# Performance work log

Hardware: AMD Instinct MI355X
Metric: run time of the kernel (lower is better)

The kernel has to match this reference:

```python
import jax, jax.numpy as jnp
import numpy as np

H = 16        # heads
DH = 64       # dim_head
DM = 1024     # query_dim = context_dim
INNER = H * DH


def setup_inputs() -> dict:
    key = jax.random.key(0)
    ks = jax.random.split(key, 5)
    s = 0.02
    queries = jax.random.normal(ks[0], (2, 2048, DM), dtype=jnp.float32)
    Wq = jax.random.normal(ks[1], (DM, INNER), dtype=jnp.float32) * s
    Wkv = jax.random.normal(ks[2], (DM, 2 * INNER), dtype=jnp.float32) * s
    Wo = jax.random.normal(ks[3], (INNER, DM), dtype=jnp.float32) * s
    bo = jax.random.normal(ks[4], (DM,), dtype=jnp.float32) * s
    return {"queries": queries, "Wq": Wq, "Wkv": Wkv, "Wo": Wo, "bo": bo}


def reference(queries, Wq, Wkv, Wo, bo):
    b, n, _ = queries.shape
    scale = DH ** -0.5
    q = queries @ Wq                       # [b, n, inner]
    kv = queries @ Wkv                     # self-attention: context = queries
    k, v = jnp.split(kv, 2, axis=-1)
    # b n (h d) -> b h n d
    split_heads = lambda t: t.reshape(b, n, H, DH).transpose(0, 2, 1, 3)
    q, k, v = map(split_heads, (q, k, v))
    sim = jnp.einsum('bhid,bhjd->bhij', q, k) * scale
    attn = jax.nn.softmax(sim, axis=-1)    # dropout is identity (p=0 / eval)
    out = jnp.einsum('bhij,bhjd->bhid', attn, v)
    out = out.transpose(0, 2, 1, 3).reshape(b, n, INNER)
    return out @ Wo + bo
```

## Files before the change

### kernel.cpp

```cpp
#include <hip/hip_runtime.h>
#include <math.h>
#include <stdint.h>

typedef _Float16 half8v __attribute__((ext_vector_type(8)));
typedef _Float16 half4v __attribute__((ext_vector_type(4)));
typedef _Float16 half2v __attribute__((ext_vector_type(2)));
typedef __fp16 fp16x2 __attribute__((ext_vector_type(2)));
typedef float floatx4 __attribute__((ext_vector_type(4)));

#define MFMA16(a, b, c) __builtin_amdgcn_mfma_f32_16x16x32_f16(a, b, c, 0, 0, 0)

#define QSCALE 0.18033688011112f

__device__ __forceinline__ void gld_lds16(const void* g, void* l) {
  __builtin_amdgcn_global_load_lds(
      (const __attribute__((address_space(1))) uint32_t*)(uintptr_t)g,
      (__attribute__((address_space(3))) uint32_t*)(uintptr_t)l, 16, 0, 0);
}

__device__ __forceinline__ half2v pk16(float a, float b) {
  fp16x2 t = __builtin_amdgcn_cvt_pkrtz(a, b);
  return __builtin_bit_cast(half2v, t);
}

__global__ __launch_bounds__(256) void prep(
    const float* __restrict__ X, const float* __restrict__ Wq,
    const float* __restrict__ Wkv, const float* __restrict__ Wo,
    _Float16* __restrict__ X16, _Float16* __restrict__ WqkvT,
    _Float16* __restrict__ WoT)
{
  __shared__ alignas(16) _Float16 Tt[64 * 68];
  const int bid = blockIdx.x;
  if (bid < 2048) {
    size_t gid = (size_t)bid * 256 + threadIdx.x;
    const float4* src = (const float4*)(X) + gid * 2;
    float4 a = src[0], b = src[1];
    half8v h;
    h[0]=(_Float16)a.x; h[1]=(_Float16)a.y; h[2]=(_Float16)a.z; h[3]=(_Float16)a.w;
    h[4]=(_Float16)b.x; h[5]=(_Float16)b.y; h[6]=(_Float16)b.z; h[7]=(_Float16)b.w;
    *((half8v*)X16 + gid) = h;
    return;
  }
  int b = bid - 2048;
  const float* src; _Float16* dst; int N, tk, tn;
  if (b < 256)      { src = Wq;  dst = WqkvT;                 N = 1024; tk = b & 15;        tn = b >> 4; }
  else if (b < 768) { src = Wkv; dst = WqkvT + (size_t)1024 * 1024; N = 2048; tk = (b - 256) & 15; tn = (b - 256) >> 4; }
  else              { src = Wo;  dst = WoT;                   N = 1024; tk = (b - 768) & 15; tn = (b - 768) >> 4; }

  const int t = threadIdx.x;
  {
    int kg = t >> 4, ng = t & 15;
    const float* sp = src + (size_t)(tk * 64 + kg * 4) * N + tn * 64 + ng * 4;
    float4 r0 = *(const float4*)(sp);
    float4 r1 = *(const float4*)(sp + N);
    float4 r2 = *(const float4*)(sp + 2 * N);
    float4 r3 = *(const float4*)(sp + 3 * N);
    half4v h;
    h[0]=(_Float16)r0.x; h[1]=(_Float16)r1.x; h[2]=(_Float16)r2.x; h[3]=(_Float16)r3.x;
    *(half4v*)&Tt[(ng * 4 + 0) * 68 + kg * 4] = h;
    h[0]=(_Float16)r0.y; h[1]=(_Float16)r1.y; h[2]=(_Float16)r2.y; h[3]=(_Float16)r3.y;
    *(half4v*)&Tt[(ng * 4 + 1) * 68 + kg * 4] = h;
    h[0]=(_Float16)r0.z; h[1]=(_Float16)r1.z; h[2]=(_Float16)r2.z; h[3]=(_Float16)r3.z;
    *(half4v*)&Tt[(ng * 4 + 2) * 68 + kg * 4] = h;
    h[0]=(_Float16)r0.w; h[1]=(_Float16)r1.w; h[2]=(_Float16)r2.w; h[3]=(_Float16)r3.w;
    *(half4v*)&Tt[(ng * 4 + 3) * 68 + kg * 4] = h;
  }
  __syncthreads();
  #pragma unroll
  for (int i = 0; i < 2; i++) {
    int idx = t + i * 256;
    int nl = idx >> 3, k8 = (idx & 7) * 8;
    half8v v = *(half8v*)&Tt[nl * 68 + k8];
    *(half8v*)(dst + (size_t)(tn * 64 + nl) * 1024 + tk * 64 + k8) = v;
  }
}

__global__ __launch_bounds__(256) void qkv_gemm(
    const _Float16* __restrict__ X16, const _Float16* __restrict__ WqkvT,
    _Float16* __restrict__ q_ws, _Float16* __restrict__ k_ws,
    _Float16* __restrict__ vT_ws)
{
  constexpr int K = 1024;
  __shared__ alignas(16) _Float16 Tt[128 * 136];
  _Float16* As = Tt;
  _Float16* Bs = Tt + 4096;

  const int m0 = blockIdx.x * 128;
  const int n0 = blockIdx.y * 128;

  const int tid  = threadIdx.x;
  const int wave = tid >> 6, lane = tid & 63;
  const int qd = lane >> 4, l15 = lane & 15;
  const int wr = (wave >> 1) * 64, wc = (wave & 1) * 64;
  const int r0i = tid >> 2, c0 = (tid & 3) * 8;

  floatx4 acc[4][4] = {};

  for (int k0 = 0; k0 < K; k0 += 32) {
    gld_lds16(X16 + (size_t)(m0 + r0i) * K + k0 + c0, &As[tid * 8]);
    gld_lds16(X16 + (size_t)(m0 + 64 + r0i) * K + k0 + c0, &As[(tid + 256) * 8]);
    gld_lds16(WqkvT + (size_t)(n0 + r0i) * K + k0 + c0, &Bs[tid * 8]);
    gld_lds16(WqkvT + (size_t)(n0 + 64 + r0i) * K + k0 + c0, &Bs[(tid + 256) * 8]);
    __syncthreads();
    half8v a[4], b[4];
    #pragma unroll
    for (int it = 0; it < 4; it++)
      a[it] = *(half8v*)&As[(wr + it * 16 + l15) * 32 + qd * 8];
    #pragma unroll
    for (int jt = 0; jt < 4; jt++)
      b[jt] = *(half8v*)&Bs[(wc + jt * 16 + l15) * 32 + qd * 8];
    #pragma unroll
    for (int it = 0; it < 4; it++)
      #pragma unroll
      for (int jt = 0; jt < 4; jt++)
        acc[it][jt] = MFMA16(a[it], b[jt], acc[it][jt]);
    __syncthreads();
  }

  if (n0 < 2048) {
    #pragma unroll
    for (int it = 0; it < 4; it++) {
      #pragma unroll
      for (int jt = 0; jt < 4; jt++) {
        #pragma unroll
        for (int r = 0; r < 4; r++) {
          int m = m0 + wr + it * 16 + qd * 4 + r;
          int n = n0 + wc + jt * 16 + l15;
          float val = acc[it][jt][r];
          int bb = m >> 11, nn = m & 2047;
          if (n0 < 1024) {
            int h = n >> 6, d = n & 63;
            q_ws[(((size_t)bb * 16 + h) * 2048 + nn) * 64 + d] = (_Float16)(val * QSCALE);
          } else {
            int c = n - 1024, h = c >> 6, d = c & 63;
            k_ws[(((size_t)bb * 16 + h) * 2048 + nn) * 64 + d] = (_Float16)val;
          }
        }
      }
    }
  } else {
    #pragma unroll
    for (int it = 0; it < 4; it++) {
      #pragma unroll
      for (int jt = 0; jt < 4; jt++) {
        #pragma unroll
        for (int r = 0; r < 4; r++) {
          int ml = wr + it * 16 + qd * 4 + r;
          int nl = wc + jt * 16 + l15;
          Tt[nl * 136 + ml] = (_Float16)acc[it][jt][r];
        }
      }
    }
    __syncthreads();
    int row = tid >> 1;
    int mh  = (tid & 1) * 64;
    int c   = (n0 - 2048) + row;
    int bb  = m0 >> 11;
    int nnb = (m0 & 2047) + mh;
    _Float16* dstp =
        vT_ws + (((size_t)bb * 16 + (c >> 6)) * 64 + (c & 63)) * 2048 + nnb;
    #pragma unroll
    for (int i = 0; i < 8; i++)
      *(half8v*)(dstp + i * 8) = *(half8v*)&Tt[row * 136 + mh + i * 8];
  }
}

__device__ __forceinline__ int swz(int row, int blk) {
  return row * 64 + ((blk ^ (row & 7)) << 3);
}

__global__ __launch_bounds__(128, 2) void attn_kernel(
    const _Float16* __restrict__ q_ws, const _Float16* __restrict__ k_ws,
    const _Float16* __restrict__ vT_ws, _Float16* __restrict__ aout)
{
  constexpr int N = 2048;
  __shared__ alignas(16) _Float16 Qs[64 * 64];
  __shared__ alignas(16) _Float16 Ks[2][64 * 64];
  __shared__ alignas(16) _Float16 Vts[2][64 * 64];

  const int id = blockIdx.x;
  const int bh = ((id >> 8) << 3) | (id & 7);
  const int qt = (id >> 3) & 31;

  const _Float16* Qp = q_ws + (size_t)bh * N * 64;
  const _Float16* Kp = k_ws + (size_t)bh * N * 64;
  const _Float16* Vp = vT_ws + (size_t)bh * 64 * N;

  const int tid = threadIdx.x, wave = tid >> 6, lane = tid & 63;
  const int qd = lane >> 4, l15 = lane & 15;
  const int q0 = qt * 64;
  const int wbase = wave * 32;

  #pragma unroll
  for (int i = 0; i < 4; i++) {
    int idx = tid + i * 128;
    int r = idx >> 3, cb = (idx ^ r) & 7;
    gld_lds16(Qp + (size_t)(q0 + r) * 64 + cb * 8, &Qs[idx * 8]);
    gld_lds16(Kp + (size_t)r * 64 + cb * 8, &Ks[0][idx * 8]);
    gld_lds16(Vp + (size_t)r * N + cb * 8, &Vts[0][idx * 8]);
  }
  __syncthreads();

  half8v qf[2][2];
  #pragma unroll
  for (int m = 0; m < 2; m++)
    #pragma unroll
    for (int ks = 0; ks < 2; ks++)
      qf[m][ks] = *(half8v*)&Qs[swz(wbase + m * 16 + l15, ks * 4 + qd)];

  floatx4 o[2][4] = {};
  float lsum[2] = {};

  int p = 0;
  for (int kv0 = 0; kv0 < N; kv0 += 64) {
    const bool more = (kv0 + 64) < N;
    if (more) {
      int kvn = kv0 + 64;
      #pragma unroll
      for (int i = 0; i < 4; i++) {
        int idx = tid + i * 128;
        int r = idx >> 3, cb = (idx ^ r) & 7;
        gld_lds16(Kp + (size_t)(kvn + r) * 64 + cb * 8, &Ks[p ^ 1][idx * 8]);
        gld_lds16(Vp + (size_t)r * N + kvn + cb * 8, &Vts[p ^ 1][idx * 8]);
      }
    }

    floatx4 s[4][2] = {};
    #pragma unroll
    for (int ks = 0; ks < 2; ks++) {
      half8v kf[4];
      #pragma unroll
      for (int nt = 0; nt < 4; nt++)
        kf[nt] = *(half8v*)&Ks[p][swz(nt * 16 + l15, ks * 4 + qd)];
      #pragma unroll
      for (int nt = 0; nt < 4; nt++)
        #pragma unroll
        for (int m = 0; m < 2; m++)
          s[nt][m] = MFMA16(kf[nt], qf[m][ks], s[nt][m]);
    }

    #pragma unroll
    for (int m = 0; m < 2; m++) {
      #pragma unroll
      for (int nt = 0; nt < 4; nt++) {
        float p0 = __builtin_amdgcn_exp2f(s[nt][m][0]);
        float p1 = __builtin_amdgcn_exp2f(s[nt][m][1]);
        float p2 = __builtin_amdgcn_exp2f(s[nt][m][2]);
        float p3 = __builtin_amdgcn_exp2f(s[nt][m][3]);
        lsum[m] += (p0 + p1) + (p2 + p3);
        half2v h01 = pk16(p0, p1);
        half2v h23 = pk16(p2, p3);
        half4v pk;
        pk[0] = h01[0]; pk[1] = h01[1]; pk[2] = h23[0]; pk[3] = h23[1];
        *(half4v*)&Qs[swz(wbase + m * 16 + l15, 2 * nt + (qd >> 1)) +
                      (qd & 1) * 4] = pk;
      }
    }

    #pragma unroll
    for (int ks = 0; ks < 2; ks++) {
      half8v pf[2], vf[4];
      #pragma unroll
      for (int m = 0; m < 2; m++)
        pf[m] = *(half8v*)&Qs[swz(wbase + m * 16 + l15, 4 * ks + qd)];
      #pragma unroll
      for (int nt = 0; nt < 4; nt++)
        vf[nt] = *(half8v*)&Vts[p][swz(nt * 16 + l15, 4 * ks + qd)];
      #pragma unroll
      for (int m = 0; m < 2; m++)
        #pragma unroll
        for (int nt = 0; nt < 4; nt++)
          o[m][nt] = MFMA16(pf[m], vf[nt], o[m][nt]);
    }

    if (more) __syncthreads();
    p ^= 1;
  }

  #pragma unroll
  for (int m = 0; m < 2; m++) {
    lsum[m] += __shfl_xor(lsum[m], 16);
    lsum[m] += __shfl_xor(lsum[m], 32);
  }

  const int bb = bh >> 4, hh = bh & 15;
  #pragma unroll
  for (int m = 0; m < 2; m++) {
    #pragma unroll
    for (int r = 0; r < 4; r++) {
      float inv = 1.0f / __shfl(lsum[m], qd * 4 + r);
      int n = q0 + wbase + m * 16 + qd * 4 + r;
      #pragma unroll
      for (int dt = 0; dt < 4; dt++) {
        int d = dt * 16 + l15;
        aout[((size_t)(bb * 2048 + n)) * 1024 + hh * 64 + d] =
            (_Float16)(o[m][dt][r] * inv);
      }
    }
  }
}

__global__ __launch_bounds__(256) void out_gemm(
    const _Float16* __restrict__ A, const _Float16* __restrict__ WoT,
    const float* __restrict__ bo, float* __restrict__ Out)
{
  constexpr int K = 1024;
  __shared__ alignas(16) _Float16 As[64 * 32];
  __shared__ alignas(16) _Float16 Bs[128 * 32];

  const int m0 = blockIdx.x * 64;
  const int n0 = blockIdx.y * 128;
  const int tid = threadIdx.x;
  const int wave = tid >> 6, lane = tid & 63;
  const int qd = lane >> 4, l15 = lane & 15;
  const int wr = (wave >> 1) * 32, wc = (wave & 1) * 64;
  const int r0i = tid >> 2, c0 = (tid & 3) * 8;

  floatx4 acc[2][4] = {};

  for (int k0 = 0; k0 < K; k0 += 32) {
    gld_lds16(A + (size_t)(m0 + r0i) * K + k0 + c0, &As[tid * 8]);
    gld_lds16(WoT + (size_t)(n0 + r0i) * K + k0 + c0, &Bs[tid * 8]);
    gld_lds16(WoT + (size_t)(n0 + 64 + r0i) * K + k0 + c0, &Bs[(tid + 256) * 8]);
    __syncthreads();
    half8v a[2], b[4];
    #pragma unroll
    for (int it = 0; it < 2; it++)
      a[it] = *(half8v*)&As[(wr + it * 16 + l15) * 32 + qd * 8];
    #pragma unroll
    for (int jt = 0; jt < 4; jt++)
      b[jt] = *(half8v*)&Bs[(wc + jt * 16 + l15) * 32 + qd * 8];
    #pragma unroll
    for (int it = 0; it < 2; it++)
      #pragma unroll
      for (int jt = 0; jt < 4; jt++)
        acc[it][jt] = MFMA16(a[it], b[jt], acc[it][jt]);
    __syncthreads();
  }

  #pragma unroll
  for (int it = 0; it < 2; it++) {
    #pragma unroll
    for (int jt = 0; jt < 4; jt++) {
      int n = n0 + wc + jt * 16 + l15;
      float bias = bo[n];
      #pragma unroll
      for (int r = 0; r < 4; r++) {
        int m = m0 + wr + it * 16 + qd * 4 + r;
        Out[(size_t)m * 1024 + n] = acc[it][jt][r] + bias;
      }
    }
  }
}

extern "C" void kernel_launch(void* const* d_in, const int* in_sizes, int n_in,
                              void* d_out, int out_size, void* d_ws, size_t ws_size,
                              hipStream_t stream) {
  const float* X   = (const float*)d_in[0];
  const float* Wq  = (const float*)d_in[1];
  const float* Wkv = (const float*)d_in[2];
  const float* Wo  = (const float*)d_in[3];
  const float* bo  = (const float*)d_in[4];
  float* out = (float*)d_out;

  const size_t M4 = (size_t)4 * 1024 * 1024;
  _Float16* q_ws   = (_Float16*)d_ws;
  _Float16* k_ws   = q_ws + M4;
  _Float16* vT_ws  = k_ws + M4;
  _Float16* X16    = vT_ws + M4;
  _Float16* WqkvT  = X16 + M4;
  _Float16* WoT    = WqkvT + (size_t)3 * 1024 * 1024;
  _Float16* aout   = X16;

  prep<<<3072, 256, 0, stream>>>(X, Wq, Wkv, Wo, X16, WqkvT, WoT);
  qkv_gemm<<<dim3(32, 24), 256, 0, stream>>>(X16, WqkvT, q_ws, k_ws, vT_ws);
  attn_kernel<<<1024, 128, 0, stream>>>(q_ws, k_ws, vT_ws, aout);
  out_gemm<<<dim3(64, 8), 256, 0, stream>>>(aout, WoT, bo, out);
}
```

Before: 190.3 us.

## Fuse all four stages into one persistent kernel with grid barriers

Replaces the four separate launches (prep, QKV GEMM, attention, output GEMM) with one persistent kernel of 512 blocks. The stages are separated by atomic-counter grid barriers, and each stage's tiles are mapped onto those blocks. The attention stage now uses 256-thread blocks covering 128 queries each, so 512 blocks replace the previous 1024 of 128 threads. This is meant to remove inter-kernel launch gaps and tail effects. In exchange, the QKV GEMM runs 768 tiles over 512 blocks, which gives an uneven second wave, and it relies on all 512 blocks being co-resident for the spin barrier to be safe.

Result: slower. 389.0 us (+104.4%).

```diff
diff --git a/kernel.cpp b/kernel.cpp
--- a/kernel.cpp
+++ b/kernel.cpp
@@ -23,331 +23,339 @@
   return __builtin_bit_cast(half2v, t);
 }
 
-__global__ __launch_bounds__(256) void prep(
+__device__ __forceinline__ int swz(int row, int blk) {
+  return row * 64 + ((blk ^ (row & 7)) << 3);
+}
+
+__device__ int g_bar;
+
+__device__ __forceinline__ void grid_barrier(int target) {
+  __syncthreads();
+  if (threadIdx.x == 0) {
+    __hip_atomic_fetch_add(&g_bar, 1, __ATOMIC_ACQ_REL,
+                           __HIP_MEMORY_SCOPE_AGENT);
+    while (__hip_atomic_load(&g_bar, __ATOMIC_ACQUIRE,
+                             __HIP_MEMORY_SCOPE_AGENT) < target)
+      __builtin_amdgcn_s_sleep(16);
+  }
+  __syncthreads();
+}
+
+__global__ __launch_bounds__(256, 2) void mega(
     const float* __restrict__ X, const float* __restrict__ Wq,
     const float* __restrict__ Wkv, const float* __restrict__ Wo,
+    const float* __restrict__ bo,
     _Float16* __restrict__ X16, _Float16* __restrict__ WqkvT,
-    _Float16* __restrict__ WoT)
+    _Float16* __restrict__ WoT,
+    _Float16* __restrict__ q_ws, _Float16* __restrict__ k_ws,
+    _Float16* __restrict__ vT_ws,
+    _Float16* __restrict__ aout, float* __restrict__ Out)
 {
-  __shared__ alignas(16) _Float16 Tt[64 * 68];
+  __shared__ alignas(16) _Float16 pool[24576];
   const int bid = blockIdx.x;
-  if (bid < 2048) {
-    size_t gid = (size_t)bid * 256 + threadIdx.x;
-    const float4* src = (const float4*)(X) + gid * 2;
-    float4 a = src[0], b = src[1];
-    half8v h;
-    h[0]=(_Float16)a.x; h[1]=(_Float16)a.y; h[2]=(_Float16)a.z; h[3]=(_Float16)a.w;
-    h[4]=(_Float16)b.x; h[5]=(_Float16)b.y; h[6]=(_Float16)b.z; h[7]=(_Float16)b.w;
-    *((half8v*)X16 + gid) = h;
-    return;
-  }
-  int b = bid - 2048;
-  const float* src; _Float16* dst; int N, tk, tn;
-  if (b < 256)      { src = Wq;  dst = WqkvT;                 N = 1024; tk = b & 15;        tn = b >> 4; }
-  else if (b < 768) { src = Wkv; dst = WqkvT + (size_t)1024 * 1024; N = 2048; tk = (b - 256) & 15; tn = (b - 256) >> 4; }
-  else              { src = Wo;  dst = WoT;                   N = 1024; tk = (b - 768) & 15; tn = (b - 768) >> 4; }
-
-  const int t = threadIdx.x;
-  {
-    int kg = t >> 4, ng = t & 15;
-    const float* sp = src + (size_t)(tk * 64 + kg * 4) * N + tn * 64 + ng * 4;
-    float4 r0 = *(const float4*)(sp);
-    float4 r1 = *(const float4*)(sp + N);
-    float4 r2 = *(const float4*)(sp + 2 * N);
-    float4 r3 = *(const float4*)(sp + 3 * N);
-    half4v h;
-    h[0]=(_Float16)r0.x; h[1]=(_Float16)r1.x; h[2]=(_Float16)r2.x; h[3]=(_Float16)r3.x;
-    *(half4v*)&Tt[(ng * 4 + 0) * 68 + kg * 4] = h;
-    h[0]=(_Float16)r0.y; h[1]=(_Float16)r1.y; h[2]=(_Float16)r2.y; h[3]=(_Float16)r3.y;
-    *(half4v*)&Tt[(ng * 4 + 1) * 68 + kg * 4] = h;
-    h[0]=(_Float16)r0.z; h[1]=(_Float16)r1.z; h[2]=(_Float16)r2.z; h[3]=(_Float16)r3.z;
-    *(half4v*)&Tt[(ng * 4 + 2) * 68 + kg * 4] = h;
-    h[0]=(_Float16)r0.w; h[1]=(_Float16)r1.w; h[2]=(_Float16)r2.w; h[3]=(_Float16)r3.w;
-    *(half4v*)&Tt[(ng * 4 + 3) * 68 + kg * 4] = h;
-  }
-  __syncthreads();
-  #pragma unroll
-  for (int i = 0; i < 2; i++) {
-    int idx = t + i * 256;
-    int nl = idx >> 3, k8 = (idx & 7) * 8;
-    half8v v = *(half8v*)&Tt[nl * 68 + k8];
-    *(half8v*)(dst + (size_t)(tn * 64 + nl) * 1024 + tk * 64 + k8) = v;
-  }
-}
-
-__global__ __launch_bounds__(256) void qkv_gemm(
-    const _Float16* __restrict__ X16, const _Float16* __restrict__ WqkvT,
-    _Float16* __restrict__ q_ws, _Float16* __restrict__ k_ws,
-    _Float16* __restrict__ vT_ws)
-{
-  constexpr int K = 1024;
-  __shared__ alignas(16) _Float16 Tt[128 * 136];
-  _Float16* As = Tt;
-  _Float16* Bs = Tt + 4096;
-
-  const int m0 = blockIdx.x * 128;
-  const int n0 = blockIdx.y * 128;
-
-  const int tid  = threadIdx.x;
-  const int wave = tid >> 6, lane = tid & 63;
-  const int qd = lane >> 4, l15 = lane & 15;
-  const int wr = (wave >> 1) * 64, wc = (wave & 1) * 64;
-  const int r0i = tid >> 2, c0 = (tid & 3) * 8;
-
-  floatx4 acc[4][4] = {};
-
-  for (int k0 = 0; k0 < K; k0 += 32) {
-    gld_lds16(X16 + (size_t)(m0 + r0i) * K + k0 + c0, &As[tid * 8]);
-    gld_lds16(X16 + (size_t)(m0 + 64 + r0i) * K + k0 + c0, &As[(tid + 256) * 8]);
-    gld_lds16(WqkvT + (size_t)(n0 + r0i) * K + k0 + c0, &Bs[tid * 8]);
-    gld_lds16(WqkvT + (size_t)(n0 + 64 + r0i) * K + k0 + c0, &Bs[(tid + 256) * 8]);
-    __syncthreads();
-    half8v a[4], b[4];
-    #pragma unroll
-    for (int it = 0; it < 4; it++)
-      a[it] = *(half8v*)&As[(wr + it * 16 + l15) * 32 + qd * 8];
-    #pragma unroll
-    for (int jt = 0; jt < 4; jt++)
-      b[jt] = *(half8v*)&Bs[(wc + jt * 16 + l15) * 32 + qd * 8];
-    #pragma unroll
-    for (int it = 0; it < 4; it++)
-      #pragma unroll
-      for (int jt = 0; jt < 4; jt++)
-        acc[it][jt] = MFMA16(a[it], b[jt], acc[it][jt]);
-    __syncthreads();
-  }
-
-  if (n0 < 2048) {
-    #pragma unroll
-    for (int it = 0; it < 4; it++) {
-      #pragma unroll
-      for (int jt = 0; jt < 4; jt++) {
-        #pragma unroll
-        for (int r = 0; r < 4; r++) {
-          int m = m0 + wr + it * 16 + qd * 4 + r;
-          int n = n0 + wc + jt * 16 + l15;
-          float val = acc[it][jt][r];
-          int bb = m >> 11, nn = m & 2047;
-          if (n0 < 1024) {
-            int h = n >> 6, d = n & 63;
-            q_ws[(((size_t)bb * 16 + h) * 2048 + nn) * 64 + d] = (_Float16)(val * QSCALE);
-          } else {
-            int c = n - 1024, h = c >> 6, d = c & 63;
-            k_ws[(((size_t)bb * 16 + h) * 2048 + nn) * 64 + d] = (_Float16)val;
-          }
-        }
-      }
-    }
-  } else {
-    #pragma unroll
-    for (int it = 0; it < 4; it++) {
-      #pragma unroll
-      for (int jt = 0; jt < 4; jt++) {
-        #pragma unroll
-        for (int r = 0; r < 4; r++) {
-          int ml = wr + it * 16 + qd * 4 + r;
-          int nl = wc + jt * 16 + l15;
-          Tt[nl * 136 + ml] = (_Float16)acc[it][jt][r];
-        }
-      }
-    }
-    __syncthreads();
-    int row = tid >> 1;
-    int mh  = (tid & 1) * 64;
-    int c   = (n0 - 2048) + row;
-    int bb  = m0 >> 11;
-    int nnb = (m0 & 2047) + mh;
-    _Float16* dstp =
-        vT_ws + (((size_t)bb * 16 + (c >> 6)) * 64 + (c & 63)) * 2048 + nnb;
-    #pragma unroll
-    for (int i = 0; i < 8; i++)
-      *(half8v*)(dstp + i * 8) = *(half8v*)&Tt[row * 136 + mh + i * 8];
-  }
-}
-
-__device__ __forceinline__ int swz(int row, int blk) {
-  return row * 64 + ((blk ^ (row & 7)) << 3);
-}
-
-__global__ __launch_bounds__(128, 2) void attn_kernel(
-    const _Float16* __restrict__ q_ws, const _Float16* __restrict__ k_ws,
-    const _Float16* __restrict__ vT_ws, _Float16* __restrict__ aout)
-{
-  constexpr int N = 2048;
-  __shared__ alignas(16) _Float16 Qs[64 * 64];
-  __shared__ alignas(16) _Float16 Ks[2][64 * 64];
-  __shared__ alignas(16) _Float16 Vts[2][64 * 64];
-
-  const int id = blockIdx.x;
-  const int bh = ((id >> 8) << 3) | (id & 7);
-  const int qt = (id >> 3) & 31;
-
-  const _Float16* Qp = q_ws + (size_t)bh * N * 64;
-  const _Float16* Kp = k_ws + (size_t)bh * N * 64;
-  const _Float16* Vp = vT_ws + (size_t)bh * 64 * N;
-
-  const int tid = threadIdx.x, wave = tid >> 6, lane = tid & 63;
-  const int qd = lane >> 4, l15 = lane & 15;
-  const int q0 = qt * 64;
-  const int wbase = wave * 32;
-
-  #pragma unroll
-  for (int i = 0; i < 4; i++) {
-    int idx = tid + i * 128;
-    int r = idx >> 3, cb = (idx ^ r) & 7;
-    gld_lds16(Qp + (size_t)(q0 + r) * 64 + cb * 8, &Qs[idx * 8]);
-    gld_lds16(Kp + (size_t)r * 64 + cb * 8, &Ks[0][idx * 8]);
-    gld_lds16(Vp + (size_t)r * N + cb * 8, &Vts[0][idx * 8]);
-  }
-  __syncthreads();
-
-  half8v qf[2][2];
-  #pragma unroll
-  for (int m = 0; m < 2; m++)
-    #pragma unroll
-    for (int ks = 0; ks < 2; ks++)
-      qf[m][ks] = *(half8v*)&Qs[swz(wbase + m * 16 + l15, ks * 4 + qd)];
-
-  floatx4 o[2][4] = {};
-  float lsum[2] = {};
-
-  int p = 0;
-  for (int kv0 = 0; kv0 < N; kv0 += 64) {
-    const bool more = (kv0 + 64) < N;
-    if (more) {
-      int kvn = kv0 + 64;
-      #pragma unroll
-      for (int i = 0; i < 4; i++) {
-        int idx = tid + i * 128;
-        int r = idx >> 3, cb = (idx ^ r) & 7;
-        gld_lds16(Kp + (size_t)(kvn + r) * 64 + cb * 8, &Ks[p ^ 1][idx * 8]);
-        gld_lds16(Vp + (size_t)r * N + kvn + cb * 8, &Vts[p ^ 1][idx * 8]);
-      }
-    }
-
-    floatx4 s[4][2] = {};
-    #pragma unroll
-    for (int ks = 0; ks < 2; ks++) {
-      half8v kf[4];
-      #pragma unroll
-      for (int nt = 0; nt < 4; nt++)
-        kf[nt] = *(half8v*)&Ks[p][swz(nt * 16 + l15, ks * 4 + qd)];
-      #pragma unroll
-      for (int nt = 0; nt < 4; nt++)
-        #pragma unroll
-        for (int m = 0; m < 2; m++)
-          s[nt][m] = MFMA16(kf[nt], qf[m][ks], s[nt][m]);
-    }
-
-    #pragma unroll
-    for (int m = 0; m < 2; m++) {
-      #pragma unroll
-      for (int nt = 0; nt < 4; nt++) {
-        float p0 = __builtin_amdgcn_exp2f(s[nt][m][0]);
-        float p1 = __builtin_amdgcn_exp2f(s[nt][m][1]);
-        float p2 = __builtin_amdgcn_exp2f(s[nt][m][2]);
-        float p3 = __builtin_amdgcn_exp2f(s[nt][m][3]);
-        lsum[m] += (p0 + p1) + (p2 + p3);
-        half2v h01 = pk16(p0, p1);
-        half2v h23 = pk16(p2, p3);
-        half4v pk;
-        pk[0] = h01[0]; pk[1] = h01[1]; pk[2] = h23[0]; pk[3] = h23[1];
-        *(half4v*)&Qs[swz(wbase + m * 16 + l15, 2 * nt + (qd >> 1)) +
-                      (qd & 1) * 4] = pk;
-      }
-    }
-
-    #pragma unroll
-    for (int ks = 0; ks < 2; ks++) {
-      half8v pf[2], vf[4];
-      #pragma unroll
-      for (int m = 0; m < 2; m++)
-        pf[m] = *(half8v*)&Qs[swz(wbase + m * 16 + l15, 4 * ks + qd)];
-      #pragma unroll
-      for (int nt = 0; nt < 4; nt++)
-        vf[nt] = *(half8v*)&Vts[p][swz(nt * 16 + l15, 4 * ks + qd)];
-      #pragma unroll
-      for (int m = 0; m < 2; m++)
-        #pragma unroll
-        for (int nt = 0; nt < 4; nt++)
-          o[m][nt] = MFMA16(pf[m], vf[nt], o[m][nt]);
-    }
-
-    if (more) __syncthreads();
-    p ^= 1;
-  }
-
-  #pragma unroll
-  for (int m = 0; m < 2; m++) {
-    lsum[m] += __shfl_xor(lsum[m], 16);
-    lsum[m] += __shfl_xor(lsum[m], 32);
-  }
-
-  const int bb = bh >> 4, hh = bh & 15;
-  #pragma unroll
-  for (int m = 0; m < 2; m++) {
-    #pragma unroll
-    for (int r = 0; r < 4; r++) {
-      float inv = 1.0f / __shfl(lsum[m], qd * 4 + r);
-      int n = q0 + wbase + m * 16 + qd * 4 + r;
-      #pragma unroll
-      for (int dt = 0; dt < 4; dt++) {
-        int d = dt * 16 + l15;
-        aout[((size_t)(bb * 2048 + n)) * 1024 + hh * 64 + d] =
-            (_Float16)(o[m][dt][r] * inv);
-      }
-    }
-  }
-}
-
-__global__ __launch_bounds__(256) void out_gemm(
-    const _Float16* __restrict__ A, const _Float16* __restrict__ WoT,
-    const float* __restrict__ bo, float* __restrict__ Out)
-{
-  constexpr int K = 1024;
-  __shared__ alignas(16) _Float16 As[64 * 32];
-  __shared__ alignas(16) _Float16 Bs[128 * 32];
-
-  const int m0 = blockIdx.x * 64;
-  const int n0 = blockIdx.y * 128;
   const int tid = threadIdx.x;
   const int wave = tid >> 6, lane = tid & 63;
   const int qd = lane >> 4, l15 = lane & 15;
-  const int wr = (wave >> 1) * 32, wc = (wave & 1) * 64;
-  const int r0i = tid >> 2, c0 = (tid & 3) * 8;
-
-  floatx4 acc[2][4] = {};
-
-  for (int k0 = 0; k0 < K; k0 += 32) {
-    gld_lds16(A + (size_t)(m0 + r0i) * K + k0 + c0, &As[tid * 8]);
-    gld_lds16(WoT + (size_t)(n0 + r0i) * K + k0 + c0, &Bs[tid * 8]);
-    gld_lds16(WoT + (size_t)(n0 + 64 + r0i) * K + k0 + c0, &Bs[(tid + 256) * 8]);
+
+  for (int j = bid; j < 3072; j += 512) {
+    if (j < 2048) {
+      size_t gid = (size_t)j * 256 + tid;
+      const float4* src = (const float4*)X + gid * 2;
+      float4 a = src[0], b = src[1];
+      half8v h;
+      h[0]=(_Float16)a.x; h[1]=(_Float16)a.y; h[2]=(_Float16)a.z; h[3]=(_Float16)a.w;
+      h[4]=(_Float16)b.x; h[5]=(_Float16)b.y; h[6]=(_Float16)b.z; h[7]=(_Float16)b.w;
+      *((half8v*)X16 + gid) = h;
+    } else {
+      int b = j - 2048;
+      const float* src; _Float16* dst; int N, tk, tn;
+      if (b < 256)      { src = Wq;  dst = WqkvT;                       N = 1024; tk = b & 15;        tn = b >> 4; }
+      else if (b < 768) { src = Wkv; dst = WqkvT + (size_t)1024 * 1024; N = 2048; tk = (b - 256) & 15; tn = (b - 256) >> 4; }
+      else              { src = Wo;  dst = WoT;                         N = 1024; tk = (b - 768) & 15; tn = (b - 768) >> 4; }
+      __syncthreads();
+      {
+        int kg = tid >> 4, ng = tid & 15;
+        const float* sp = src + (size_t)(tk * 64 + kg * 4) * N + tn * 64 + ng * 4;
+        float4 r0 = *(const float4*)(sp);
+        float4 r1 = *(const float4*)(sp + N);
+        float4 r2 = *(const float4*)(sp + 2 * N);
+        float4 r3 = *(const float4*)(sp + 3 * N);
+        half4v h;
+        h[0]=(_Float16)r0.x; h[1]=(_Float16)r1.x; h[2]=(_Float16)r2.x; h[3]=(_Float16)r3.x;
+        *(half4v*)&pool[(ng * 4 + 0) * 68 + kg * 4] = h;
+        h[0]=(_Float16)r0.y; h[1]=(_Float16)r1.y; h[2]=(_Float16)r2.y; h[3]=(_Float16)r3.y;
+        *(half4v*)&pool[(ng * 4 + 1) * 68 + kg * 4] = h;
+        h[0]=(_Float16)r0.z; h[1]=(_Float16)r1.z; h[2]=(_Float16)r2.z; h[3]=(_Float16)r3.z;
+        *(half4v*)&pool[(ng * 4 + 2) * 68 + kg * 4] = h;
+        h[0]=(_Float16)r0.w; h[1]=(_Float16)r1.w; h[2]=(_Float16)r2.w; h[3]=(_Float16)r3.w;
+        *(half4v*)&pool[(ng * 4 + 3) * 68 + kg * 4] = h;
+      }
+      __syncthreads();
+      #pragma unroll
+      for (int i = 0; i < 2; i++) {
+        int idx = tid + i * 256;
+        int nl = idx >> 3, k8 = (idx & 7) * 8;
+        half8v v = *(half8v*)&pool[nl * 68 + k8];
+        *(half8v*)(dst + (size_t)(tn * 64 + nl) * 1024 + tk * 64 + k8) = v;
+      }
+    }
+  }
+  grid_barrier(512);
+
+  for (int jj = bid; jj < 768; jj += 512) {
     __syncthreads();
-    half8v a[2], b[4];
-    #pragma unroll
-    for (int it = 0; it < 2; it++)
-      a[it] = *(half8v*)&As[(wr + it * 16 + l15) * 32 + qd * 8];
-    #pragma unroll
-    for (int jt = 0; jt < 4; jt++)
-      b[jt] = *(half8v*)&Bs[(wc + jt * 16 + l15) * 32 + qd * 8];
-    #pragma unroll
-    for (int it = 0; it < 2; it++)
+    constexpr int K = 1024;
+    _Float16* As = pool;
+    _Float16* Bs = pool + 4096;
+    const int m0 = (jj & 31) * 128;
+    const int n0 = (jj >> 5) * 128;
+    const int wr = (wave >> 1) * 64, wc = (wave & 1) * 64;
+    const int r0i = tid >> 2, c0 = (tid & 3) * 8;
+
+    floatx4 acc[4][4] = {};
+    for (int k0 = 0; k0 < K; k0 += 32) {
+      gld_lds16(X16 + (size_t)(m0 + r0i) * K + k0 + c0, &As[tid * 8]);
+      gld_lds16(X16 + (size_t)(m0 + 64 + r0i) * K + k0 + c0, &As[(tid + 256) * 8]);
+      gld_lds16(WqkvT + (size_t)(n0 + r0i) * K + k0 + c0, &Bs[tid * 8]);
+      gld_lds16(WqkvT + (size_t)(n0 + 64 + r0i) * K + k0 + c0, &Bs[(tid + 256) * 8]);
+      __syncthreads();
+      half8v a[4], b[4];
+      #pragma unroll
+      for (int it = 0; it < 4; it++)
+        a[it] = *(half8v*)&As[(wr + it * 16 + l15) * 32 + qd * 8];
       #pragma unroll
       for (int jt = 0; jt < 4; jt++)
-        acc[it][jt] = MFMA16(a[it], b[jt], acc[it][jt]);
+        b[jt] = *(half8v*)&Bs[(wc + jt * 16 + l15) * 32 + qd * 8];
+      #pragma unroll
+      for (int it = 0; it < 4; it++)
+        #pragma unroll
+        for (int jt = 0; jt < 4; jt++)
+          acc[it][jt] = MFMA16(a[it], b[jt], acc[it][jt]);
+      __syncthreads();
+    }
+
+    if (n0 < 2048) {
+      #pragma unroll
+      for (int it = 0; it < 4; it++) {
+        #pragma unroll
+        for (int jt = 0; jt < 4; jt++) {
+          #pragma unroll
+          for (int r = 0; r < 4; r++) {
+            int m = m0 + wr + it * 16 + qd * 4 + r;
+            int n = n0 + wc + jt * 16 + l15;
+            float val = acc[it][jt][r];
+            int bb = m >> 11, nn = m & 2047;
+            if (n0 < 1024) {
+              int h = n >> 6, d = n & 63;
+              q_ws[(((size_t)bb * 16 + h) * 2048 + nn) * 64 + d] = (_Float16)(val * QSCALE);
+            } else {
+              int c = n - 1024, h = c >> 6, d = c & 63;
+              k_ws[(((size_t)bb * 16 + h) * 2048 + nn) * 64 + d] = (_Float16)val;
+            }
+          }
+        }
+      }
+    } else {
+      #pragma unroll
+      for (int it = 0; it < 4; it++) {
+        #pragma unroll
+        for (int jt = 0; jt < 4; jt++) {
+          #pragma unroll
+          for (int r = 0; r < 4; r++) {
+            int ml = wr + it * 16 + qd * 4 + r;
+            int nl = wc + jt * 16 + l15;
+            pool[nl * 136 + ml] = (_Float16)acc[it][jt][r];
+          }
+        }
+      }
+      __syncthreads();
+      int row = tid >> 1;
+      int mh  = (tid & 1) * 64;
+      int c   = (n0 - 2048) + row;
+      int bb  = m0 >> 11;
+      int nnb = (m0 & 2047) + mh;
+      _Float16* dstp =
+          vT_ws + (((size_t)bb * 16 + (c >> 6)) * 64 + (c & 63)) * 2048 + nnb;
+      #pragma unroll
+      for (int i = 0; i < 8; i++)
+        *(half8v*)(dstp + i * 8) = *(half8v*)&pool[row * 136 + mh + i * 8];
+    }
+  }
+  grid_barrier(1024);
+
+  {
+    constexpr int N = 2048;
+    _Float16* Qs  = pool;
+    _Float16* Ks  = pool + 8192;
+    _Float16* Vts = pool + 16384;
+
+    const int bh = ((bid >> 7) << 3) | (bid & 7);
+    const int qt = (bid >> 3) & 15;
+    const int q0 = qt * 128;
+    const int wbase = wave * 32;
+
+    const _Float16* Qp = q_ws + (size_t)bh * N * 64;
+    const _Float16* Kp = k_ws + (size_t)bh * N * 64;
+    const _Float16* Vp = vT_ws + (size_t)bh * 64 * N;
+
+    #pragma unroll
+    for (int i = 0; i < 4; i++) {
+      int idx = tid + i * 256;
+      int r = idx >> 3, cb = (idx ^ r) & 7;
+      gld_lds16(Qp + (size_t)(q0 + r) * 64 + cb * 8, &Qs[idx * 8]);
+    }
+    #pragma unroll
+    for (int i = 0; i < 2; i++) {
+      int idx = tid + i * 256;
+      int r = idx >> 3, cb = (idx ^ r) & 7;
+      gld_lds16(Kp + (size_t)r * 64 + cb * 8, &Ks[idx * 8]);
+      gld_lds16(Vp + (size_t)r * N + cb * 8, &Vts[idx * 8]);
+    }
     __syncthreads();
-  }
-
-  #pragma unroll
-  for (int it = 0; it < 2; it++) {
-    #pragma unroll
-    for (int jt = 0; jt < 4; jt++) {
-      int n = n0 + wc + jt * 16 + l15;
-      float bias = bo[n];
+
+    half8v qf[2][2];
+    #pragma unroll
+    for (int m = 0; m < 2; m++)
+      #pragma unroll
+      for (int ks = 0; ks < 2; ks++)
+        qf[m][ks] = *(half8v*)&Qs[swz(wbase + m * 16 + l15, ks * 4 + qd)];
+
+    floatx4 o[2][4] = {};
+    float lsum[2] = {};
+
+    int p = 0;
+    for (int kv0 = 0; kv0 < N; kv0 += 64) {
+      const bool more = (kv0 + 64) < N;
+      if (more) {
+        int kvn = kv0 + 64;
+        #pragma unroll
+        for (int i = 0; i < 2; i++) {
+          int idx = tid + i * 256;
+          int r = idx >> 3, cb = (idx ^ r) & 7;
+          gld_lds16(Kp + (size_t)(kvn + r) * 64 + cb * 8,
+                    &Ks[(p ^ 1) * 4096 + idx * 8]);
+          gld_lds16(Vp + (size_t)r * N + kvn + cb * 8,
+                    &Vts[(p ^ 1) * 4096 + idx * 8]);
+        }
+      }
+
+      floatx4 s[4][2] = {};
+      #pragma unroll
+      for (int ks = 0; ks < 2; ks++) {
+        half8v kf[4];
+        #pragma unroll
+        for (int nt = 0; nt < 4; nt++)
+          kf[nt] = *(half8v*)&Ks[p * 4096 + swz(nt * 16 + l15, ks * 4 + qd)];
+        #pragma unroll
+        for (int nt = 0; nt < 4; nt++)
+          #pragma unroll
+          for (int m = 0; m < 2; m++)
+            s[nt][m] = MFMA16(kf[nt], qf[m][ks], s[nt][m]);
+      }
+
+      #pragma unroll
+      for (int m = 0; m < 2; m++) {
+        #pragma unroll
+        for (int nt = 0; nt < 4; nt++) {
+          float p0 = __builtin_amdgcn_exp2f(s[nt][m][0]);
+          float p1 = __builtin_amdgcn_exp2f(s[nt][m][1]);
+          float p2 = __builtin_amdgcn_exp2f(s[nt][m][2]);
+          float p3 = __builtin_amdgcn_exp2f(s[nt][m][3]);
+          lsum[m] += (p0 + p1) + (p2 + p3);
+          half2v h01 = pk16(p0, p1);
+          half2v h23 = pk16(p2, p3);
+          half4v pk;
+          pk[0] = h01[0]; pk[1] = h01[1]; pk[2] = h23[0]; pk[3] = h23[1];
+          *(half4v*)&Qs[swz(wbase + m * 16 + l15, 2 * nt + (qd >> 1)) +
+                        (qd & 1) * 4] = pk;
+        }
+      }
+
+      #pragma unroll
+      for (int ks = 0; ks < 2; ks++) {
+        half8v pf[2], vf[4];
+        #pragma unroll
+        for (int m = 0; m < 2; m++)
+          pf[m] = *(half8v*)&Qs[swz(wbase + m * 16 + l15, 4 * ks + qd)];
+        #pragma unroll
+        for (int nt = 0; nt < 4; nt++)
+          vf[nt] = *(half8v*)&Vts[p * 4096 + swz(nt * 16 + l15, 4 * ks + qd)];
+        #pragma unroll
+        for (int m = 0; m < 2; m++)
+          #pragma unroll
+          for (int nt = 0; nt < 4; nt++)
+            o[m][nt] = MFMA16(pf[m], vf[nt], o[m][nt]);
+      }
+
+      if (more) __syncthreads();
+      p ^= 1;
+    }
+
+    #pragma unroll
+    for (int m = 0; m < 2; m++) {
+      lsum[m] += __shfl_xor(lsum[m], 16);
+      lsum[m] += __shfl_xor(lsum[m], 32);
+    }
+
+    const int bb = bh >> 4, hh = bh & 15;
+    #pragma unroll
+    for (int m = 0; m < 2; m++) {
       #pragma unroll
       for (int r = 0; r < 4; r++) {
-        int m = m0 + wr + it * 16 + qd * 4 + r;
-        Out[(size_t)m * 1024 + n] = acc[it][jt][r] + bias;
+        float inv = 1.0f / __shfl(lsum[m], qd * 4 + r);
+        int n = q0 + wbase + m * 16 + qd * 4 + r;
+        #pragma unroll
+        for (int dt = 0; dt < 4; dt++) {
+          int d = dt * 16 + l15;
+          aout[((size_t)(bb * 2048 + n)) * 1024 + hh * 64 + d] =
+              (_Float16)(o[m][dt][r] * inv);
+        }
+      }
+    }
+  }
+  grid_barrier(1536);
+
+  {
+    constexpr int K = 1024;
+    _Float16* As = pool;
+    _Float16* Bs = pool + 2048;
+    const int m0 = (bid & 63) * 64;
+    const int n0 = (bid >> 6) * 128;
+    const int wr = (wave >> 1) * 32, wc = (wave & 1) * 64;
+    const int r0i = tid >> 2, c0 = (tid & 3) * 8;
+
+    floatx4 acc[2][4] = {};
+    for (int k0 = 0; k0 < K; k0 += 32) {
+      gld_lds16(aout + (size_t)(m0 + r0i) * K + k0 + c0, &As[tid * 8]);
+      gld_lds16(WoT + (size_t)(n0 + r0i) * K + k0 + c0, &Bs[tid * 8]);
+      gld_lds16(WoT + (size_t)(n0 + 64 + r0i) * K + k0 + c0, &Bs[(tid + 256) * 8]);
+      __syncthreads();
+      half8v a[2], b[4];
+      #pragma unroll
+      for (int it = 0; it < 2; it++)
+        a[it] = *(half8v*)&As[(wr + it * 16 + l15) * 32 + qd * 8];
+      #pragma unroll
+      for (int jt = 0; jt < 4; jt++)
+        b[jt] = *(half8v*)&Bs[(wc + jt * 16 + l15) * 32 + qd * 8];
+      #pragma unroll
+      for (int it = 0; it < 2; it++)
+        #pragma unroll
+        for (int jt = 0; jt < 4; jt++)
+          acc[it][jt] = MFMA16(a[it], b[jt], acc[it][jt]);
+      __syncthreads();
+    }
+
+    #pragma unroll
+    for (int it = 0; it < 2; it++) {
+      #pragma unroll
+      for (int jt = 0; jt < 4; jt++) {
+        int n = n0 + wc + jt * 16 + l15;
+        float bias = bo[n];
+        #pragma unroll
+        for (int r = 0; r < 4; r++) {
+          int m = m0 + wr + it * 16 + qd * 4 + r;
+          Out[(size_t)m * 1024 + n] = acc[it][jt][r] + bias;
+        }
       }
     }
   }
@@ -372,8 +380,10 @@
   _Float16* WoT    = WqkvT + (size_t)3 * 1024 * 1024;
   _Float16* aout   = X16;
 
-  prep<<<3072, 256, 0, stream>>>(X, Wq, Wkv, Wo, X16, WqkvT, WoT);
-  qkv_gemm<<<dim3(32, 24), 256, 0, stream>>>(X16, WqkvT, q_ws, k_ws, vT_ws);
-  attn_kernel<<<1024, 128, 0, stream>>>(q_ws, k_ws, vT_ws, aout);
-  out_gemm<<<dim3(64, 8), 256, 0, stream>>>(aout, WoT, bo, out);
-}
+  void* bar_addr = nullptr;
+  hipGetSymbolAddress(&bar_addr, HIP_SYMBOL(g_bar));
+  hipMemsetAsync(bar_addr, 0, sizeof(int), stream);
+
+  mega<<<512, 256, 0, stream>>>(X, Wq, Wkv, Wo, bo, X16, WqkvT, WoT,
+                                q_ws, k_ws, vT_ws, aout, out);
+}
```
